# Optimization experiments

Measured on AMD Instinct MI355X. Metric: run time of the kernel, lower is better.

Reference implementation:

```python
import jax, jax.numpy as jnp
import numpy as np

B, S, T, F, H = 128, 512, 128, 64, 1024


def _lstm_cell(x, h, c, Wih, Whh, bih, bhh):
    # PyTorch gate order: i, f, g, o
    g = x @ Wih.T + h @ Whh.T + bih + bhh  # [B, 4H]
    i, f, gg, o = jnp.split(g, 4, axis=-1)
    c2 = jax.nn.sigmoid(f) * c + jax.nn.sigmoid(i) * jnp.tanh(gg)
    h2 = jax.nn.sigmoid(o) * jnp.tanh(c2)
    return h2, c2


def setup_inputs() -> dict:
    key = jax.random.key(0)
    ks = jax.random.split(key, 12)
    sc = 1.0 / np.sqrt(H)  # torch LSTM init scale
    f32 = jnp.float32
    return {
        "source": jax.random.normal(ks[0], (B, S, F), f32),
        "target": jax.random.normal(ks[1], (B, T, 1), f32),
        "enc_Wih": jax.random.uniform(ks[2], (4 * H, F), f32, -sc, sc),
        "enc_Whh": jax.random.uniform(ks[3], (4 * H, H), f32, -sc, sc),
        "enc_bih": jax.random.uniform(ks[4], (4 * H,), f32, -sc, sc),
        "enc_bhh": jax.random.uniform(ks[5], (4 * H,), f32, -sc, sc),
        "dec_Wih": jax.random.uniform(ks[6], (4 * H, 1), f32, -sc, sc),
        "dec_Whh": jax.random.uniform(ks[7], (4 * H, H), f32, -sc, sc),
        "dec_bih": jax.random.uniform(ks[8], (4 * H,), f32, -sc, sc),
        "dec_bhh": jax.random.uniform(ks[9], (4 * H,), f32, -sc, sc),
        "fc_W": jax.random.uniform(ks[10], (1, H), f32, -sc, sc),
        "fc_b": jax.random.uniform(ks[11], (1,), f32, -sc, sc),
    }


def reference(source, target, enc_Wih, enc_Whh, enc_bih, enc_bhh,
              dec_Wih, dec_Whh, dec_bih, dec_bhh, fc_W, fc_b):
    b = source.shape[0]
    t_len = target.shape[1]
    hdim = enc_Whh.shape[1]
    dt = source.dtype

    # ---- Encoder: run LSTM over source, keep final (h, c) ----
    h0 = jnp.zeros((b, hdim), dt)
    c0 = jnp.zeros((b, hdim), dt)

    def enc_step(carry, x_t):
        h, c = carry
        h, c = _lstm_cell(x_t, h, c, enc_Wih, enc_Whh, enc_bih, enc_bhh)
        return (h, c), None

    (h, c), _ = jax.lax.scan(enc_step, (h0, c0), source.transpose(1, 0, 2))

    x0 = target[:, 0, :]  # [B, 1]

    def dec_step(carry, _):
        x, hh, cc = carry
        hh, cc = _lstm_cell(x, hh, cc, dec_Wih, dec_Whh, dec_bih, dec_bhh)
        pred = hh @ fc_W.T + fc_b  # [B, 1]
        return (pred, hh, cc), pred

    _, preds = jax.lax.scan(dec_step, (x0, h, c), None, length=t_len - 1)
    # outputs[:, 0, :] stays zero (loop starts at t=1 in the original)
    outputs = jnp.concatenate(
        [jnp.zeros((b, 1, 1), dt), preds.transpose(1, 0, 2)], axis=1
    )
    return outputs
```

## Files before the change

### kernel.cpp

```cpp
#include <hip/hip_runtime.h>
#include <hip/hip_fp16.h>
#include <math.h>

#define BB 128
#define SS 512
#define TT 128
#define FF 64
#define HH 1024

#define NBT 8
#define NJB 32
#define NBLK 256
#define NTHR 256

typedef _Float16 half8 __attribute__((ext_vector_type(8)));
typedef float    f32x4 __attribute__((ext_vector_type(4)));
typedef unsigned long long u64;

__device__ __forceinline__ float rcpf(float x){ return __builtin_amdgcn_rcpf(x); }
__device__ __forceinline__ float sigm(float x){ return rcpf(1.f + __expf(-x)); }
__device__ __forceinline__ float tfast(float x){
  float a = fabsf(x);
  float e = __expf(-2.f*a);
  float t = (1.f - e) * rcpf(1.f + e);
  return copysignf(t, x);
}

__device__ __forceinline__ u64 aload64(const u64* p){
  return __hip_atomic_load(p, __ATOMIC_RELAXED, __HIP_MEMORY_SCOPE_AGENT);
}
__device__ __forceinline__ float aloadf(const float* p){
  return __hip_atomic_load(p, __ATOMIC_RELAXED, __HIP_MEMORY_SCOPE_AGENT);
}
__device__ __forceinline__ void astoref(float* p, float v){
  __hip_atomic_store(p, v, __ATOMIC_RELAXED, __HIP_MEMORY_SCOPE_AGENT);
}
__device__ __forceinline__ void astoreu(unsigned* p, unsigned v){
  __hip_atomic_store(p, v, __ATOMIC_RELAXED, __HIP_MEMORY_SCOPE_AGENT);
}

__device__ __forceinline__ void bar_arrive(unsigned* flags, int jblk, unsigned* barno){
  asm volatile("s_waitcnt vmcnt(0)" ::: "memory");
  __syncthreads();
  ++(*barno);
  if (threadIdx.x == 0) astoreu(&flags[jblk], *barno);
}
__device__ __forceinline__ void bar_wait(const unsigned* flags, unsigned barno){
  if (threadIdx.x < 32){
    while (__hip_atomic_load(&flags[threadIdx.x], __ATOMIC_RELAXED,
                             __HIP_MEMORY_SCOPE_AGENT) < barno) {}
  }
  __syncthreads();
}

__global__ __launch_bounds__(256) void cvt_plain(const float* __restrict__ s,
                                                 ushort* __restrict__ d, int n){
  for (int i = blockIdx.x*256 + threadIdx.x; i < n; i += gridDim.x*256)
    d[i] = __half_as_ushort(__float2half(s[i]));
}
__global__ __launch_bounds__(256) void cvt_src(const float* __restrict__ s,
                                               ushort* __restrict__ d){
  for (int i = blockIdx.x*256 + threadIdx.x; i < BB*SS*FF; i += gridDim.x*256){
    int f = i & 63, st = (i >> 6) & 511, b = i >> 15;
    d[(((size_t)st*8 + (f>>3))*128 + b)*8 + (f&7)] = __half_as_ushort(__float2half(s[i]));
  }
}

__global__ __launch_bounds__(NTHR, 1) void seq_kernel(
  const float*  __restrict__ tgt,
  const _Float16* __restrict__ src16T,
  const _Float16* __restrict__ wih16,
  const _Float16* __restrict__ ewhh16,
  const _Float16* __restrict__ dwhh16,
  const float* __restrict__ ebih, const float* __restrict__ ebhh,
  const float* __restrict__ dWih,
  const float* __restrict__ dbih, const float* __restrict__ dbhh,
  const float* __restrict__ fcW, const float* __restrict__ fcb,
  float* __restrict__ out, ushort* h16u, float* ppsl, unsigned* barflags)
{
  __shared__ float Ct4[4][16][132];
  __shared__ float xacc[2][16];
  __shared__ float predsum[16];

  const int tid = threadIdx.x;
  const int wk  = tid >> 6;
  const int l   = tid & 63;
  const int la  = l & 15, lq = l >> 4;
  const int btile = blockIdx.x >> 5;
  const int jblk  = blockIdx.x & 31;
  const int m = tid & 15, q = tid >> 4;
  unsigned* flags = barflags + btile*32;
  unsigned barno = 0;

  half8 Bh[64];
  #pragma unroll
  for (int kc = 0; kc < 8; kc++)
    #pragma unroll
    for (int nt = 0; nt < 8; nt++){
      size_t grow = (size_t)((nt>>1)*HH + jblk*32 + (nt&1)*16 + la);
      Bh[kc*8+nt] = *(const half8*)(ewhh16 + grow*HH + wk*256 + kc*32 + lq*8);
    }
  half8 Bx[8];
  if (wk < 2)
    #pragma unroll
    for (int nt = 0; nt < 8; nt++){
      size_t grow = (size_t)((nt>>1)*HH + jblk*32 + (nt&1)*16 + la);
      Bx[nt] = *(const half8*)(wih16 + grow*FF + wk*32 + lq*8);
    }

  float ebv[8], wxv[8], fcwv[2];
  #pragma unroll
  for (int g = 0; g < 4; g++)
    #pragma unroll
    for (int u = 0; u < 2; u++){
      int jg = jblk*32 + 2*q + u;
      ebv[g*2+u] = ebih[g*HH + jg] + ebhh[g*HH + jg];
      wxv[g*2+u] = 0.f;
    }
  fcwv[0] = fcwv[1] = 0.f;
  const float fcb0v = fcb[0];

  if (jblk == 0 && tid < 16) out[(size_t)(btile*16 + tid)*TT] = 0.f;
  bar_arrive(flags, jblk, &barno);

  float cc0 = 0.f, cc1 = 0.f;

  for (int t = 0; t < SS + TT - 1; t++){
    const bool enc = (t < SS);
    f32x4 acc[8];
    #pragma unroll
    for (int nt = 0; nt < 8; nt++)
      #pragma unroll
      for (int r = 0; r < 4; r++) acc[nt][r] = 0.f;

    if (t == SS){
      #pragma unroll
      for (int kc = 0; kc < 8; kc++)
        #pragma unroll
        for (int nt = 0; nt < 8; nt++){
          size_t grow = (size_t)((nt>>1)*HH + jblk*32 + (nt&1)*16 + la);
          Bh[kc*8+nt] = *(const half8*)(dwhh16 + grow*HH + wk*256 + kc*32 + lq*8);
        }
      #pragma unroll
      for (int g = 0; g < 4; g++)
        #pragma unroll
        for (int u = 0; u < 2; u++){
          int jg = jblk*32 + 2*q + u;
          ebv[g*2+u] = dbih[g*HH + jg] + dbhh[g*HH + jg];
          wxv[g*2+u] = dWih[g*HH + jg];
        }
      fcwv[0] = fcW[jblk*32 + 2*q];
      fcwv[1] = fcW[jblk*32 + 2*q + 1];
    }

    if (enc && wk < 2){
      half8 xa = *(const half8*)(src16T +
                   (((size_t)t*8 + wk*4 + lq)*128 + btile*16 + la)*8);
      #pragma unroll
      for (int nt = 0; nt < 8; nt++)
        acc[nt] = __builtin_amdgcn_mfma_f32_16x16x32_f16(xa, Bx[nt], acc[nt], 0,0,0);
    }

    bar_wait(flags, barno);

    float pv0 = 0.f, pv1 = 0.f;
    if (!enc && t > SS){
      const float* pp = ppsl + ((size_t)(((t+1)&1)*NBT + btile)*NJB)*16;
      pv0 = aloadf(pp + (size_t)q*16 + m);
      pv1 = aloadf(pp + (size_t)(q+16)*16 + m);
    }

    if (t > 0){
      u64 w0[8], w1[8];
      const ushort* hb = h16u + ((size_t)((t&1)*128 + wk*32)*128)*8;
      #pragma unroll
      for (int kc = 0; kc < 8; kc++){
        const u64* p = (const u64*)(hb + ((size_t)(kc*4+lq)*128 + btile*16 + la)*8);
        w0[kc] = aload64(p); w1[kc] = aload64(p+1);
      }
      #pragma unroll
      for (int kc = 0; kc < 8; kc++){
        union { u64 qq[2]; half8 v; } ua;
        ua.qq[0] = w0[kc]; ua.qq[1] = w1[kc];
        #pragma unroll
        for (int nt = 0; nt < 8; nt++)
          acc[nt] = __builtin_amdgcn_mfma_f32_16x16x32_f16(ua.v, Bh[kc*8+nt], acc[nt], 0,0,0);
      }
    }

    if (tid < 16) predsum[tid] = 0.f;
    if (tid >= 16 && tid < 32) xacc[(t+1)&1][tid-16] = 0.f;
    #pragma unroll
    for (int nt = 0; nt < 8; nt++)
      #pragma unroll
      for (int r = 0; r < 4; r++)
        Ct4[wk][lq*4 + r][nt*16 + la] = acc[nt][r];
    float xr = 0.f;
    if (!enc){
      if (t == SS) xr = tgt[(size_t)(btile*16 + m)*TT];
      else atomicAdd(&xacc[t&1][m], pv0 + pv1);
    }
    __syncthreads();
    if (!enc && t > SS){
      xr = xacc[t&1][m] + fcb0v;
      if (jblk == 0 && tid < 16)
        out[(size_t)(btile*16 + tid)*TT + (t - SS)] = xacc[t&1][tid] + fcb0v;
    }

    float gv[8];
    #pragma unroll
    for (int g = 0; g < 4; g++)
      #pragma unroll
      for (int u = 0; u < 2; u++){
        int n = g*32 + 2*q + u;
        float s2 = ((Ct4[0][m][n] + Ct4[1][m][n]) + (Ct4[2][m][n] + Ct4[3][m][n]))
                 + ebv[g*2+u];
        if (!enc) s2 += xr * wxv[g*2+u];
        gv[g*2+u] = s2;
      }
    float h2[2];
    #pragma unroll
    for (int u = 0; u < 2; u++){
      float si = sigm(gv[0+u]), sf = sigm(gv[2+u]), so = sigm(gv[6+u]);
      float tg = tfast(gv[4+u]);
      float c = u ? cc1 : cc0;
      c = sf*c + si*tg;
      if (u) cc1 = c; else cc0 = c;
      h2[u] = so * tfast(c);
    }
    {
      int o = jblk*4 + (q >> 2);
      unsigned hv = (unsigned)__half_as_ushort(__float2half(h2[0]))
                  | ((unsigned)__half_as_ushort(__float2half(h2[1])) << 16);
      astoreu((unsigned*)(h16u + ((size_t)(((t+1)&1)*128 + o)*128 + btile*16 + m)*8
                          + (q&3)*2), hv);
    }
    if (!enc){
      atomicAdd(&predsum[m], h2[0]*fcwv[0] + h2[1]*fcwv[1]);
      __syncthreads();
      if (tid < 16)
        astoref(ppsl + (((size_t)(t&1)*NBT + btile)*NJB + jblk)*16 + tid, predsum[tid]);
    }
    bar_arrive(flags, jblk, &barno);
  }

  if (jblk == 0){
    bar_wait(flags, barno);
    const float* pp = ppsl + ((size_t)btile*NJB)*16;
    float v = aloadf(pp + (size_t)q*16 + m) + aloadf(pp + (size_t)(q+16)*16 + m);
    atomicAdd(&xacc[1][m], v);
    __syncthreads();
    if (tid < 16)
      out[(size_t)(btile*16 + tid)*TT + (TT-1)] = xacc[1][tid] + fcb0v;
  }
}

extern "C" void kernel_launch(void* const* d_in, const int* in_sizes, int n_in,
                              void* d_out, int out_size, void* d_ws, size_t ws_size,
                              hipStream_t stream){
  (void)in_sizes; (void)n_in; (void)out_size; (void)ws_size;
  const float* src  = (const float*)d_in[0];
  const float* tgt  = (const float*)d_in[1];
  const float* eWih = (const float*)d_in[2];
  const float* eWhh = (const float*)d_in[3];
  const float* ebih = (const float*)d_in[4];
  const float* ebhh = (const float*)d_in[5];
  const float* dWih = (const float*)d_in[6];
  const float* dWhh = (const float*)d_in[7];
  const float* dbih = (const float*)d_in[8];
  const float* dbhh = (const float*)d_in[9];
  const float* fcW  = (const float*)d_in[10];
  const float* fcb  = (const float*)d_in[11];
  float* out = (float*)d_out;

  ushort* h16    = (ushort*)d_ws;
  ushort* src16T = h16    + 262144;
  ushort* wih16  = src16T + 4194304;
  ushort* ewhh16 = wih16  + 262144;
  ushort* dwhh16 = ewhh16 + 4194304;
  float*  ppsl   = (float*)(dwhh16 + 4194304);
  unsigned* barflags = (unsigned*)(ppsl + 8192);

  hipMemsetAsync(barflags, 0, NBT*NJB*sizeof(unsigned), stream);
  cvt_src  <<<4096, 256, 0, stream>>>(src, src16T);
  cvt_plain<<<1024, 256, 0, stream>>>(eWih, wih16,  4*HH*FF);
  cvt_plain<<<4096, 256, 0, stream>>>(eWhh, ewhh16, 4*HH*HH);
  cvt_plain<<<4096, 256, 0, stream>>>(dWhh, dwhh16, 4*HH*HH);
  seq_kernel<<<dim3(NBLK), dim3(NTHR), 0, stream>>>(
      tgt, (const _Float16*)src16T, (const _Float16*)wih16,
      (const _Float16*)ewhh16, (const _Float16*)dwhh16,
      ebih, ebhh, dWih, dbih, dbhh, fcW, fcb, out, h16, ppsl, barflags);
}
```

Before: 2.616 ms.

## Map batch tiles onto single XCDs and use XCD-local sc0 loads/stores

```diff
diff --git a/kernel.cpp b/kernel.cpp
--- a/kernel.cpp
+++ b/kernel.cpp
@@ -15,6 +15,7 @@
 
 typedef _Float16 half8 __attribute__((ext_vector_type(8)));
 typedef float    f32x4 __attribute__((ext_vector_type(4)));
+typedef unsigned uint4v __attribute__((ext_vector_type(4)));
 typedef unsigned long long u64;
 
 __device__ __forceinline__ float rcpf(float x){ return __builtin_amdgcn_rcpf(x); }
@@ -32,11 +33,27 @@
 __device__ __forceinline__ float aloadf(const float* p){
   return __hip_atomic_load(p, __ATOMIC_RELAXED, __HIP_MEMORY_SCOPE_AGENT);
 }
+__device__ __forceinline__ unsigned aloadu(const unsigned* p){
+  return __hip_atomic_load(p, __ATOMIC_RELAXED, __HIP_MEMORY_SCOPE_AGENT);
+}
 __device__ __forceinline__ void astoref(float* p, float v){
   __hip_atomic_store(p, v, __ATOMIC_RELAXED, __HIP_MEMORY_SCOPE_AGENT);
 }
 __device__ __forceinline__ void astoreu(unsigned* p, unsigned v){
   __hip_atomic_store(p, v, __ATOMIC_RELAXED, __HIP_MEMORY_SCOPE_AGENT);
+}
+
+__device__ __forceinline__ void stu_sc0(unsigned* p, unsigned v){
+  asm volatile("global_store_dword %0, %1, off sc0" :: "v"(p), "v"(v) : "memory");
+}
+__device__ __forceinline__ void stf_sc0(float* p, float v){
+  asm volatile("global_store_dword %0, %1, off sc0" :: "v"(p), "v"(v) : "memory");
+}
+__device__ __forceinline__ void ld2f_issue_sc0(const float* p0, const float* p1,
+                                               float& a, float& b){
+  asm volatile("global_load_dword %0, %2, off sc0\n\t"
+               "global_load_dword %1, %3, off sc0"
+               : "=&v"(a), "=&v"(b) : "v"(p0), "v"(p1) : "memory");
 }
 
 __device__ __forceinline__ void bar_arrive(unsigned* flags, int jblk, unsigned* barno){
@@ -45,12 +62,20 @@
   ++(*barno);
   if (threadIdx.x == 0) astoreu(&flags[jblk], *barno);
 }
-__device__ __forceinline__ void bar_wait(const unsigned* flags, unsigned barno){
+__device__ __forceinline__ void bar_wait_full(const unsigned* flags, unsigned barno){
   if (threadIdx.x < 32){
     while (__hip_atomic_load(&flags[threadIdx.x], __ATOMIC_RELAXED,
                              __HIP_MEMORY_SCOPE_AGENT) < barno) {}
   }
   __syncthreads();
+}
+__device__ __forceinline__ void bar_wait_wave8(const unsigned* flags, unsigned barno, int wk){
+  int ll = threadIdx.x & 63;
+  if (ll < 8){
+    while (__hip_atomic_load(&flags[wk*8 + ll], __ATOMIC_RELAXED,
+                             __HIP_MEMORY_SCOPE_AGENT) < barno) {}
+  }
+  __builtin_amdgcn_sched_barrier(0);
 }
 
 __global__ __launch_bounds__(256) void cvt_plain(const float* __restrict__ s,
@@ -63,6 +88,205 @@
   for (int i = blockIdx.x*256 + threadIdx.x; i < BB*SS*FF; i += gridDim.x*256){
     int f = i & 63, st = (i >> 6) & 511, b = i >> 15;
     d[(((size_t)st*8 + (f>>3))*128 + b)*8 + (f&7)] = __half_as_ushort(__float2half(s[i]));
+  }
+}
+
+template<bool LOC>
+__device__ __forceinline__ void run_loop(
+  int tid, int btile, int jblk, unsigned barno,
+  const float* __restrict__ tgt,
+  const _Float16* __restrict__ src16T,
+  const _Float16* __restrict__ dwhh16,
+  const float* __restrict__ dWih,
+  const float* __restrict__ dbih, const float* __restrict__ dbhh,
+  const float* __restrict__ fcW, float fcb0v,
+  float* __restrict__ out, ushort* __restrict__ h16u,
+  float* __restrict__ ppsl, unsigned* __restrict__ flags,
+  half8 (&Bh)[64], const half8 (&Bx)[8],
+  float (&ebv)[8], float (&wxv)[8], float (&fcwv)[2],
+  float (&Ct4)[4][16][132], float (&xacc)[2][16], float (&predsum)[16])
+{
+  const int wk = tid >> 6;
+  const int l  = tid & 63;
+  const int la = l & 15, lq = l >> 4;
+  const int m = tid & 15, q = tid >> 4;
+  float cc0 = 0.f, cc1 = 0.f;
+
+  for (int t = 0; t < SS + TT - 1; t++){
+    const bool enc = (t < SS);
+    f32x4 acc[8];
+    #pragma unroll
+    for (int nt = 0; nt < 8; nt++)
+      #pragma unroll
+      for (int r = 0; r < 4; r++) acc[nt][r] = 0.f;
+
+    if (t == SS){
+      #pragma unroll
+      for (int kc = 0; kc < 8; kc++)
+        #pragma unroll
+        for (int nt = 0; nt < 8; nt++){
+          size_t grow = (size_t)((nt>>1)*HH + jblk*32 + (nt&1)*16 + la);
+          Bh[kc*8+nt] = *(const half8*)(dwhh16 + grow*HH + wk*256 + kc*32 + lq*8);
+        }
+      #pragma unroll
+      for (int g = 0; g < 4; g++)
+        #pragma unroll
+        for (int u = 0; u < 2; u++){
+          int jg = jblk*32 + 2*q + u;
+          ebv[g*2+u] = dbih[g*HH + jg] + dbhh[g*HH + jg];
+          wxv[g*2+u] = dWih[g*HH + jg];
+        }
+      fcwv[0] = fcW[jblk*32 + 2*q];
+      fcwv[1] = fcW[jblk*32 + 2*q + 1];
+    }
+
+    if (enc && wk < 2){
+      half8 xa = *(const half8*)(src16T +
+                   (((size_t)t*8 + wk*4 + lq)*128 + btile*16 + la)*8);
+      #pragma unroll
+      for (int nt = 0; nt < 8; nt++)
+        acc[nt] = __builtin_amdgcn_mfma_f32_16x16x32_f16(xa, Bx[nt], acc[nt], 0,0,0);
+    }
+
+    if (t <= SS) bar_wait_wave8(flags, barno, wk);
+    else         bar_wait_full(flags, barno);
+
+    float pv0 = 0.f, pv1 = 0.f;
+    const bool haspred = (!enc && t > SS);
+    if (haspred){
+      const float* pp = ppsl + ((size_t)(((t+1)&1)*NBT + btile)*NJB)*16;
+      if constexpr (LOC){
+        ld2f_issue_sc0(pp + (size_t)q*16 + m, pp + (size_t)(q+16)*16 + m, pv0, pv1);
+      } else {
+        pv0 = aloadf(pp + (size_t)q*16 + m);
+        pv1 = aloadf(pp + (size_t)(q+16)*16 + m);
+      }
+    }
+
+    if (t > 0){
+      const ushort* hb = h16u + ((size_t)((t&1)*8 + btile))*16384
+                       + (size_t)wk*4096 + (size_t)lq*128 + (size_t)la*8;
+      if constexpr (LOC){
+        uint4v hv[8];
+        asm volatile(
+          "global_load_dwordx4 %0, %8, off sc0\n\t"
+          "global_load_dwordx4 %1, %8, off offset:1024 sc0\n\t"
+          "global_load_dwordx4 %2, %8, off offset:2048 sc0\n\t"
+          "global_load_dwordx4 %3, %8, off offset:3072 sc0\n\t"
+          "global_load_dwordx4 %4, %9, off sc0\n\t"
+          "global_load_dwordx4 %5, %9, off offset:1024 sc0\n\t"
+          "global_load_dwordx4 %6, %9, off offset:2048 sc0\n\t"
+          "global_load_dwordx4 %7, %9, off offset:3072 sc0\n\t"
+          "s_waitcnt vmcnt(0)"
+          : "=&v"(hv[0]), "=&v"(hv[1]), "=&v"(hv[2]), "=&v"(hv[3]),
+            "=&v"(hv[4]), "=&v"(hv[5]), "=&v"(hv[6]), "=&v"(hv[7])
+          : "v"(hb), "v"(hb + 2048)
+          : "memory");
+        __builtin_amdgcn_sched_barrier(0);
+        #pragma unroll
+        for (int kc = 0; kc < 8; kc++){
+          union { uint4v u; half8 h; } ua; ua.u = hv[kc];
+          #pragma unroll
+          for (int nt = 0; nt < 8; nt++)
+            acc[nt] = __builtin_amdgcn_mfma_f32_16x16x32_f16(ua.h, Bh[kc*8+nt], acc[nt], 0,0,0);
+        }
+      } else {
+        u64 w0[8], w1[8];
+        #pragma unroll
+        for (int kc = 0; kc < 8; kc++){
+          const u64* p = (const u64*)(hb + (size_t)kc*512);
+          w0[kc] = aload64(p); w1[kc] = aload64(p+1);
+        }
+        #pragma unroll
+        for (int kc = 0; kc < 8; kc++){
+          union { u64 qq[2]; half8 v; } ua;
+          ua.qq[0] = w0[kc]; ua.qq[1] = w1[kc];
+          #pragma unroll
+          for (int nt = 0; nt < 8; nt++)
+            acc[nt] = __builtin_amdgcn_mfma_f32_16x16x32_f16(ua.v, Bh[kc*8+nt], acc[nt], 0,0,0);
+        }
+      }
+    }
+
+    if constexpr (LOC){
+      if (haspred) asm volatile("" : "+v"(pv0), "+v"(pv1));
+    }
+
+    if (tid < 16) predsum[tid] = 0.f;
+    if (tid >= 16 && tid < 32) xacc[(t+1)&1][tid-16] = 0.f;
+    #pragma unroll
+    for (int nt = 0; nt < 8; nt++)
+      #pragma unroll
+      for (int r = 0; r < 4; r++)
+        Ct4[wk][lq*4 + r][nt*16 + la] = acc[nt][r];
+    float xr = 0.f;
+    if (!enc){
+      if (t == SS) xr = tgt[(size_t)(btile*16 + m)*TT];
+      else atomicAdd(&xacc[t&1][m], pv0 + pv1);
+    }
+    __syncthreads();
+    if (!enc && t > SS){
+      xr = xacc[t&1][m] + fcb0v;
+      if (jblk == 0 && tid < 16)
+        out[(size_t)(btile*16 + tid)*TT + (t - SS)] = xacc[t&1][tid] + fcb0v;
+    }
+
+    float gv[8];
+    #pragma unroll
+    for (int g = 0; g < 4; g++)
+      #pragma unroll
+      for (int u = 0; u < 2; u++){
+        int n = g*32 + 2*q + u;
+        float s2 = ((Ct4[0][m][n] + Ct4[1][m][n]) + (Ct4[2][m][n] + Ct4[3][m][n]))
+                 + ebv[g*2+u];
+        if (!enc) s2 += xr * wxv[g*2+u];
+        gv[g*2+u] = s2;
+      }
+    float h2[2];
+    #pragma unroll
+    for (int u = 0; u < 2; u++){
+      float si = sigm(gv[0+u]), sf = sigm(gv[2+u]), so = sigm(gv[6+u]);
+      float tg = tfast(gv[4+u]);
+      float c = u ? cc1 : cc0;
+      c = sf*c + si*tg;
+      if (u) cc1 = c; else cc0 = c;
+      h2[u] = so * tfast(c);
+    }
+    {
+      int o = jblk*4 + (q >> 2);
+      unsigned hvw = (unsigned)__half_as_ushort(__float2half(h2[0]))
+                   | ((unsigned)__half_as_ushort(__float2half(h2[1])) << 16);
+      unsigned* hp = (unsigned*)(h16u + ((size_t)(((t+1)&1)*8 + btile))*16384
+                                 + ((size_t)o*16 + m)*8 + (q&3)*2);
+      if constexpr (LOC) stu_sc0(hp, hvw); else astoreu(hp, hvw);
+    }
+    if (!enc){
+      atomicAdd(&predsum[m], h2[0]*fcwv[0] + h2[1]*fcwv[1]);
+      __syncthreads();
+      if (tid < 16){
+        float* pps = ppsl + (((size_t)(t&1)*NBT + btile)*NJB + jblk)*16 + tid;
+        if constexpr (LOC) stf_sc0(pps, predsum[tid]); else astoref(pps, predsum[tid]);
+      }
+    }
+    bar_arrive(flags, jblk, &barno);
+  }
+
+  if (jblk == 0){
+    bar_wait_full(flags, barno);
+    const float* pp = ppsl + ((size_t)btile*NJB)*16;
+    float a, b;
+    if constexpr (LOC){
+      ld2f_issue_sc0(pp + (size_t)q*16 + m, pp + (size_t)(q+16)*16 + m, a, b);
+      asm volatile("s_waitcnt vmcnt(0)" ::: "memory");
+      asm volatile("" : "+v"(a), "+v"(b));
+    } else {
+      a = aloadf(pp + (size_t)q*16 + m);
+      b = aloadf(pp + (size_t)(q+16)*16 + m);
+    }
+    atomicAdd(&xacc[1][m], a + b);
+    __syncthreads();
+    if (tid < 16)
+      out[(size_t)(btile*16 + tid)*TT + (TT-1)] = xacc[1][tid] + fcb0v;
   }
 }
 
@@ -76,21 +300,21 @@
   const float* __restrict__ dWih,
   const float* __restrict__ dbih, const float* __restrict__ dbhh,
   const float* __restrict__ fcW, const float* __restrict__ fcb,
-  float* __restrict__ out, ushort* h16u, float* ppsl, unsigned* barflags)
+  float* __restrict__ out, ushort* h16u, float* ppsl, unsigned* barflags,
+  unsigned* xcdtab)
 {
   __shared__ float Ct4[4][16][132];
   __shared__ float xacc[2][16];
   __shared__ float predsum[16];
+  __shared__ int s_loc;
 
   const int tid = threadIdx.x;
   const int wk  = tid >> 6;
   const int l   = tid & 63;
   const int la  = l & 15, lq = l >> 4;
-  const int btile = blockIdx.x >> 5;
-  const int jblk  = blockIdx.x & 31;
-  const int m = tid & 15, q = tid >> 4;
-  unsigned* flags = barflags + btile*32;
-  unsigned barno = 0;
+  const int btile = blockIdx.x & 7;
+  const int jblk  = blockIdx.x >> 3;
+  const int q = tid >> 4;
 
   half8 Bh[64];
   #pragma unroll
@@ -121,138 +345,34 @@
   const float fcb0v = fcb[0];
 
   if (jblk == 0 && tid < 16) out[(size_t)(btile*16 + tid)*TT] = 0.f;
+
+  unsigned xcc;
+  asm volatile("s_getreg_b32 %0, hwreg(HW_REG_XCC_ID)" : "=s"(xcc));
+  if (tid == 0) astoreu(&xcdtab[btile*NJB + jblk], xcc + 1u);
+
+  unsigned* flags = barflags + btile*NJB;
+  unsigned barno = 0;
   bar_arrive(flags, jblk, &barno);
-
-  float cc0 = 0.f, cc1 = 0.f;
-
-  for (int t = 0; t < SS + TT - 1; t++){
-    const bool enc = (t < SS);
-    f32x4 acc[8];
-    #pragma unroll
-    for (int nt = 0; nt < 8; nt++)
-      #pragma unroll
-      for (int r = 0; r < 4; r++) acc[nt][r] = 0.f;
-
-    if (t == SS){
-      #pragma unroll
-      for (int kc = 0; kc < 8; kc++)
-        #pragma unroll
-        for (int nt = 0; nt < 8; nt++){
-          size_t grow = (size_t)((nt>>1)*HH + jblk*32 + (nt&1)*16 + la);
-          Bh[kc*8+nt] = *(const half8*)(dwhh16 + grow*HH + wk*256 + kc*32 + lq*8);
-        }
-      #pragma unroll
-      for (int g = 0; g < 4; g++)
-        #pragma unroll
-        for (int u = 0; u < 2; u++){
-          int jg = jblk*32 + 2*q + u;
-          ebv[g*2+u] = dbih[g*HH + jg] + dbhh[g*HH + jg];
-          wxv[g*2+u] = dWih[g*HH + jg];
-        }
-      fcwv[0] = fcW[jblk*32 + 2*q];
-      fcwv[1] = fcW[jblk*32 + 2*q + 1];
-    }
-
-    if (enc && wk < 2){
-      half8 xa = *(const half8*)(src16T +
-                   (((size_t)t*8 + wk*4 + lq)*128 + btile*16 + la)*8);
-      #pragma unroll
-      for (int nt = 0; nt < 8; nt++)
-        acc[nt] = __builtin_amdgcn_mfma_f32_16x16x32_f16(xa, Bx[nt], acc[nt], 0,0,0);
-    }
-
-    bar_wait(flags, barno);
-
-    float pv0 = 0.f, pv1 = 0.f;
-    if (!enc && t > SS){
-      const float* pp = ppsl + ((size_t)(((t+1)&1)*NBT + btile)*NJB)*16;
-      pv0 = aloadf(pp + (size_t)q*16 + m);
-      pv1 = aloadf(pp + (size_t)(q+16)*16 + m);
-    }
-
-    if (t > 0){
-      u64 w0[8], w1[8];
-      const ushort* hb = h16u + ((size_t)((t&1)*128 + wk*32)*128)*8;
-      #pragma unroll
-      for (int kc = 0; kc < 8; kc++){
-        const u64* p = (const u64*)(hb + ((size_t)(kc*4+lq)*128 + btile*16 + la)*8);
-        w0[kc] = aload64(p); w1[kc] = aload64(p+1);
-      }
-      #pragma unroll
-      for (int kc = 0; kc < 8; kc++){
-        union { u64 qq[2]; half8 v; } ua;
-        ua.qq[0] = w0[kc]; ua.qq[1] = w1[kc];
-        #pragma unroll
-        for (int nt = 0; nt < 8; nt++)
-          acc[nt] = __builtin_amdgcn_mfma_f32_16x16x32_f16(ua.v, Bh[kc*8+nt], acc[nt], 0,0,0);
-      }
-    }
-
-    if (tid < 16) predsum[tid] = 0.f;
-    if (tid >= 16 && tid < 32) xacc[(t+1)&1][tid-16] = 0.f;
-    #pragma unroll
-    for (int nt = 0; nt < 8; nt++)
-      #pragma unroll
-      for (int r = 0; r < 4; r++)
-        Ct4[wk][lq*4 + r][nt*16 + la] = acc[nt][r];
-    float xr = 0.f;
-    if (!enc){
-      if (t == SS) xr = tgt[(size_t)(btile*16 + m)*TT];
-      else atomicAdd(&xacc[t&1][m], pv0 + pv1);
-    }
-    __syncthreads();
-    if (!enc && t > SS){
-      xr = xacc[t&1][m] + fcb0v;
-      if (jblk == 0 && tid < 16)
-        out[(size_t)(btile*16 + tid)*TT + (t - SS)] = xacc[t&1][tid] + fcb0v;
-    }
-
-    float gv[8];
-    #pragma unroll
-    for (int g = 0; g < 4; g++)
-      #pragma unroll
-      for (int u = 0; u < 2; u++){
-        int n = g*32 + 2*q + u;
-        float s2 = ((Ct4[0][m][n] + Ct4[1][m][n]) + (Ct4[2][m][n] + Ct4[3][m][n]))
-                 + ebv[g*2+u];
-        if (!enc) s2 += xr * wxv[g*2+u];
-        gv[g*2+u] = s2;
-      }
-    float h2[2];
-    #pragma unroll
-    for (int u = 0; u < 2; u++){
-      float si = sigm(gv[0+u]), sf = sigm(gv[2+u]), so = sigm(gv[6+u]);
-      float tg = tfast(gv[4+u]);
-      float c = u ? cc1 : cc0;
-      c = sf*c + si*tg;
-      if (u) cc1 = c; else cc0 = c;
-      h2[u] = so * tfast(c);
-    }
-    {
-      int o = jblk*4 + (q >> 2);
-      unsigned hv = (unsigned)__half_as_ushort(__float2half(h2[0]))
-                  | ((unsigned)__half_as_ushort(__float2half(h2[1])) << 16);
-      astoreu((unsigned*)(h16u + ((size_t)(((t+1)&1)*128 + o)*128 + btile*16 + m)*8
-                          + (q&3)*2), hv);
-    }
-    if (!enc){
-      atomicAdd(&predsum[m], h2[0]*fcwv[0] + h2[1]*fcwv[1]);
-      __syncthreads();
-      if (tid < 16)
-        astoref(ppsl + (((size_t)(t&1)*NBT + btile)*NJB + jblk)*16 + tid, predsum[tid]);
-    }
-    bar_arrive(flags, jblk, &barno);
-  }
-
-  if (jblk == 0){
-    bar_wait(flags, barno);
-    const float* pp = ppsl + ((size_t)btile*NJB)*16;
-    float v = aloadf(pp + (size_t)q*16 + m) + aloadf(pp + (size_t)(q+16)*16 + m);
-    atomicAdd(&xacc[1][m], v);
-    __syncthreads();
-    if (tid < 16)
-      out[(size_t)(btile*16 + tid)*TT + (TT-1)] = xacc[1][tid] + fcb0v;
-  }
+  bar_wait_full(flags, barno);
+
+  if (tid < 64){
+    unsigned ent = 1u;
+    if (tid < NJB) ent = aloadu(&xcdtab[btile*NJB + tid]);
+    unsigned ref = __shfl(ent, 0, 64);
+    bool ok = (tid < NJB) ? (ent == ref && ent != 0u) : true;
+    unsigned long long bal = __ballot(ok);
+    if (tid == 0) s_loc = (bal == ~0ull) ? 1 : 0;
+  }
+  __syncthreads();
+
+  if (s_loc)
+    run_loop<true >(tid, btile, jblk, barno, tgt, src16T, dwhh16, dWih, dbih, dbhh,
+                    fcW, fcb0v, out, h16u, ppsl, flags, Bh, Bx, ebv, wxv, fcwv,
+                    Ct4, xacc, predsum);
+  else
+    run_loop<false>(tid, btile, jblk, barno, tgt, src16T, dwhh16, dWih, dbih, dbhh,
+                    fcW, fcb0v, out, h16u, ppsl, flags, Bh, Bx, ebv, wxv, fcwv,
+                    Ct4, xacc, predsum);
 }
 
 extern "C" void kernel_launch(void* const* d_in, const int* in_sizes, int n_in,
@@ -280,8 +400,9 @@
   ushort* dwhh16 = ewhh16 + 4194304;
   float*  ppsl   = (float*)(dwhh16 + 4194304);
   unsigned* barflags = (unsigned*)(ppsl + 8192);
-
-  hipMemsetAsync(barflags, 0, NBT*NJB*sizeof(unsigned), stream);
+  unsigned* xcdtab   = barflags + NBT*NJB;
+
+  hipMemsetAsync(barflags, 0, 2*NBT*NJB*sizeof(unsigned), stream);
   cvt_src  <<<4096, 256, 0, stream>>>(src, src16T);
   cvt_plain<<<1024, 256, 0, stream>>>(eWih, wih16,  4*HH*FF);
   cvt_plain<<<4096, 256, 0, stream>>>(eWhh, ewhh16, 4*HH*HH);
@@ -289,5 +410,6 @@
   seq_kernel<<<dim3(NBLK), dim3(NTHR), 0, stream>>>(
       tgt, (const _Float16*)src16T, (const _Float16*)wih16,
       (const _Float16*)ewhh16, (const _Float16*)dwhh16,
-      ebih, ebhh, dWih, dbih, dbhh, fcW, fcb, out, h16, ppsl, barflags);
-}
+      ebih, ebhh, dWih, dbih, dbhh, fcW, fcb, out, h16, ppsl, barflags,
+      xcdtab);
+}
```

After: 2.655 ms. No clear change (+1.5%).
